# Kernel tuning notes

Hardware: AMD Instinct MI355X
Metric: run time of the kernel (lower is better)

## Reference

```python
import jax, jax.numpy as jnp
import numpy as np

VAR_W = 1.0
DIST_W = 1.0
M_VAR = 0.1
M_DIST = 1.5
IGNORE = 255
C = 16  # static upper bound on instance ids (labels 1..C; 0 = background)


def setup_inputs() -> dict:
    key = jax.random.key(0)
    ks = jax.random.split(key, 6)
    shapes = [(16, 1, 1024, 1024), (16, 1, 512, 512), (16, 1, 256, 256)]
    d = {}
    for idx, s in enumerate(shapes):
        d[f"featmap{idx}"] = jax.random.normal(ks[idx], s, dtype=jnp.float32)
        d[f"gt{idx}"] = jax.random.randint(ks[3 + idx], s, 0, C + 1, dtype=jnp.int32)
    return d


def _push_pull(feats, gts):
    B = feats[0].shape[0]
    nseg = B * (C + 1)
    b_off = (jnp.arange(B, dtype=jnp.int32) * (C + 1))[:, None]  # [B,1]

    segs, valids, ffs = [], [], []
    tot_sum = jnp.zeros((nseg,), dtype=feats[0].dtype)
    tot_cnt = jnp.zeros((nseg,), dtype=feats[0].dtype)
    # pass 1: per (batch, instance) sums / counts pooled over all scales
    for f, g in zip(feats, gts):
        ff = f.reshape(B, -1)            # [B, N_s]
        gg = g.reshape(B, -1)
        valid = (gg >= 1) & (gg <= C) & (gg < IGNORE)
        lab = jnp.where(valid, gg, 0)
        seg = (lab + b_off).reshape(-1)  # [B*N_s], segment id = b*(C+1)+label
        vf = valid.reshape(-1).astype(ff.dtype)
        tot_sum = tot_sum + jax.ops.segment_sum(jnp.where(valid, ff, 0.0).reshape(-1), seg, num_segments=nseg)
        tot_cnt = tot_cnt + jax.ops.segment_sum(vf, seg, num_segments=nseg)
        segs.append(seg); valids.append(valid); ffs.append(ff)

    mean = tot_sum / jnp.maximum(tot_cnt, 1.0)  # [nseg] per-(b,instance) mean over all scales

    # pass 2: pull loss -- per-scale mean of clamp(|x - mean| - margin_var, 0)^2, summed over scales
    pull_seg = jnp.zeros((nseg,), dtype=feats[0].dtype)
    for ff, seg, valid in zip(ffs, segs, valids):
        m_pix = mean[seg].reshape(ff.shape)
        val = jnp.where(valid, jnp.square(jnp.maximum(jnp.abs(ff - m_pix) - M_VAR, 0.0)), 0.0)
        ssum = jax.ops.segment_sum(val.reshape(-1), seg, num_segments=nseg)
        scnt = jax.ops.segment_sum(valid.reshape(-1).astype(ff.dtype), seg, num_segments=nseg)
        pull_seg = pull_seg + jnp.where(scnt > 0, ssum / jnp.maximum(scnt, 1.0), 0.0)

    present = tot_cnt.reshape(B, C + 1)[:, 1:] > 0        # [B,C]
    pull_i = pull_seg.reshape(B, C + 1)[:, 1:]            # [B,C]
    n_pull = jnp.maximum(present.sum(), 1).astype(pull_i.dtype)
    pull_loss = jnp.sum(jnp.where(present, pull_i, 0.0)) / n_pull * VAR_W

    # push loss: all ordered pairs (i,j), i!=j, both present in that batch element
    m = mean.reshape(B, C + 1)[:, 1:]                     # [B,C]
    diff = jnp.abs(m[:, :, None] - m[:, None, :])         # [B,C,C]
    pv = jnp.square(jnp.maximum(2.0 * M_DIST - diff, 0.0))
    pm = present[:, :, None] & present[:, None, :] & ~jnp.eye(C, dtype=bool)[None]
    n_push = jnp.maximum(pm.sum(), 1).astype(pv.dtype)
    push_loss = jnp.sum(jnp.where(pm, pv, 0.0)) / n_push * DIST_W

    return push_loss + pull_loss


def reference(featmap0, featmap1, featmap2, gt0, gt1, gt2):
    return _push_pull([featmap0, featmap1, featmap2], [gt0, gt1, gt2])
```

## Files before the change

kernel.cpp:

```cpp
#include <hip/hip_runtime.h>


#define NSEG 272
#define M_VAR 0.1f
#define TWO_M_DIST 3.0f

__device__ __forceinline__ void gatomic_add(float* p, float v) {
  __hip_atomic_fetch_add(p, v, __ATOMIC_RELAXED, __HIP_MEMORY_SCOPE_AGENT);
}

#define GRID_BLOCKS 1008

struct Sel {
  const float4* f; const int4* g;
  int vbase, vend, stride, scale, batch;
};

__device__ __forceinline__ Sel pick(
    int b, int t,
    const float4* f0, const int4* g0,
    const float4* f1, const int4* g1,
    const float4* f2, const int4* g2) {
  Sel s;
  if (b < 768) {
    int batch = b / 48, sub = b - batch * 48;
    s.f = f0; s.g = g0; s.scale = 0; s.batch = batch;
    s.vbase = batch * 262144 + sub * 256 + t;
    s.vend  = (batch + 1) * 262144;
    s.stride = 48 * 256;
  } else if (b < 960) {
    int lb = b - 768; int batch = lb / 12, sub = lb - batch * 12;
    s.f = f1; s.g = g1; s.scale = 1; s.batch = batch;
    s.vbase = batch * 65536 + sub * 256 + t;
    s.vend  = (batch + 1) * 65536;
    s.stride = 12 * 256;
  } else {
    int lb = b - 960; int batch = lb / 3, sub = lb - batch * 3;
    s.f = f2; s.g = g2; s.scale = 2; s.batch = batch;
    s.vbase = batch * 16384 + sub * 256 + t;
    s.vend  = (batch + 1) * 16384;
    s.stride = 3 * 256;
  }
  return s;
}

__global__ __launch_bounds__(256, 4) void pass1_kernel(
    const float4* __restrict__ f0, const int4* __restrict__ g0,
    const float4* __restrict__ f1, const int4* __restrict__ g1,
    const float4* __restrict__ f2, const int4* __restrict__ g2,
    float* __restrict__ tot_sum,
    float* __restrict__ cnt)
{
  __shared__ float2 bins[17 * 256];
  const int t = threadIdx.x;
  for (int i = t; i < 17 * 256; i += 256) bins[i] = make_float2(0.f, 0.f);
  __syncthreads();

  Sel s = pick(blockIdx.x, t, f0, g0, f1, g1, f2, g2);

  for (int v = s.vbase; v < s.vend; v += s.stride) {
    float4 fv = s.f[v];
    int4   gv = s.g[v];
    {
      int idx = (int)min((unsigned)gv.x, 16u) * 256 + t;
      float2 r = bins[idx]; bins[idx] = make_float2(r.x + fv.x, r.y + 1.f);
    }
    {
      int idx = (int)min((unsigned)gv.y, 16u) * 256 + t;
      float2 r = bins[idx]; bins[idx] = make_float2(r.x + fv.y, r.y + 1.f);
    }
    {
      int idx = (int)min((unsigned)gv.z, 16u) * 256 + t;
      float2 r = bins[idx]; bins[idx] = make_float2(r.x + fv.z, r.y + 1.f);
    }
    {
      int idx = (int)min((unsigned)gv.w, 16u) * 256 + t;
      float2 r = bins[idx]; bins[idx] = make_float2(r.x + fv.w, r.y + 1.f);
    }
  }

  for (int sh = 7; sh >= 0; --sh) {
    __syncthreads();
    int off = 1 << sh;
    for (int i = t; i < 17 * off; i += 256) {
      int l = i >> sh, tt = i & (off - 1);
      int a = l * 256 + tt;
      float2 x = bins[a], y = bins[a + off];
      bins[a] = make_float2(x.x + y.x, x.y + y.y);
    }
  }
  __syncthreads();

  if (t >= 1 && t < 17) {
    float2 r = bins[t * 256];
    if (r.y != 0.f) {
      gatomic_add(&tot_sum[s.batch * 17 + t], r.x);
      gatomic_add(&cnt[s.scale * NSEG + s.batch * 17 + t], r.y);
    }
  }
}

__global__ __launch_bounds__(256) void mean_kernel(
    const float* __restrict__ tot_sum, const float* __restrict__ cnt,
    float* __restrict__ mean, float* __restrict__ tot_cnt) {
  for (int i = threadIdx.x; i < NSEG; i += 256) {
    float c = cnt[i] + cnt[NSEG + i] + cnt[2 * NSEG + i];
    tot_cnt[i] = c;
    mean[i] = tot_sum[i] / fmaxf(c, 1.f);
  }
}

__global__ __launch_bounds__(256, 8) void pass2_kernel(
    const float4* __restrict__ f0, const int4* __restrict__ g0,
    const float4* __restrict__ f1, const int4* __restrict__ g1,
    const float4* __restrict__ f2, const int4* __restrict__ g2,
    const float* __restrict__ mean,
    float* __restrict__ pull)
{
  __shared__ float bins[17 * 256];
  __shared__ float s_mean[17];
  const int t = threadIdx.x;

  Sel s = pick(blockIdx.x, t, f0, g0, f1, g1, f2, g2);

  for (int i = t; i < 17 * 256; i += 256) bins[i] = 0.f;
  if (t < 17) s_mean[t] = mean[s.batch * 17 + t];
  __syncthreads();

  for (int v = s.vbase; v < s.vend; v += s.stride) {
    float4 fv = s.f[v];
    int4   gv = s.g[v];
    {
      int l = (int)min((unsigned)gv.x, 16u);
      float d = fmaxf(fabsf(fv.x - s_mean[l]) - M_VAR, 0.f);
      bins[l * 256 + t] += d * d;
    }
    {
      int l = (int)min((unsigned)gv.y, 16u);
      float d = fmaxf(fabsf(fv.y - s_mean[l]) - M_VAR, 0.f);
      bins[l * 256 + t] += d * d;
    }
    {
      int l = (int)min((unsigned)gv.z, 16u);
      float d = fmaxf(fabsf(fv.z - s_mean[l]) - M_VAR, 0.f);
      bins[l * 256 + t] += d * d;
    }
    {
      int l = (int)min((unsigned)gv.w, 16u);
      float d = fmaxf(fabsf(fv.w - s_mean[l]) - M_VAR, 0.f);
      bins[l * 256 + t] += d * d;
    }
  }

  for (int sh = 7; sh >= 0; --sh) {
    __syncthreads();
    int off = 1 << sh;
    for (int i = t; i < 17 * off; i += 256) {
      int l = i >> sh, tt = i & (off - 1);
      bins[l * 256 + tt] += bins[l * 256 + tt + off];
    }
  }
  __syncthreads();

  if (t >= 1 && t < 17) {
    float r = bins[t * 256];
    if (r != 0.f) gatomic_add(&pull[s.scale * NSEG + s.batch * 17 + t], r);
  }
}

__global__ __launch_bounds__(256) void finalize_kernel(
    const float* __restrict__ tot_cnt, const float* __restrict__ mean,
    const float* __restrict__ cnt, const float* __restrict__ pull,
    float* __restrict__ out) {
  __shared__ float s_mean[NSEG];
  __shared__ unsigned char s_pres[NSEG];
  const int t = threadIdx.x;
  for (int i = t; i < NSEG; i += 256) {
    s_mean[i] = mean[i];
    s_pres[i] = (tot_cnt[i] > 0.f) ? 1 : 0;
  }
  __syncthreads();

  float pull_v = 0.f, pull_n = 0.f, push_v = 0.f, push_n = 0.f;

  for (int i = t; i < NSEG; i += 256) {
    int lab = i - (i / 17) * 17;
    if (lab >= 1 && s_pres[i]) {
      float ps = 0.f;
      float c0 = cnt[i];            if (c0 > 0.f) ps += pull[i] / c0;
      float c1 = cnt[NSEG + i];     if (c1 > 0.f) ps += pull[NSEG + i] / c1;
      float c2 = cnt[2 * NSEG + i]; if (c2 > 0.f) ps += pull[2 * NSEG + i] / c2;
      pull_v += ps;
      pull_n += 1.f;
    }
  }

  {
    int b = t >> 4, ii = t & 15;
    int si = b * 17 + ii + 1;
    if (s_pres[si]) {
      float mi = s_mean[si];
      for (int j = 0; j < 16; ++j) {
        if (j == ii) continue;
        int sj = b * 17 + j + 1;
        if (s_pres[sj]) {
          float d = fmaxf(TWO_M_DIST - fabsf(mi - s_mean[sj]), 0.f);
          push_v += d * d;
          push_n += 1.f;
        }
      }
    }
  }

  #pragma unroll
  for (int o = 32; o > 0; o >>= 1) {
    pull_v += __shfl_down(pull_v, o);
    pull_n += __shfl_down(pull_n, o);
    push_v += __shfl_down(push_v, o);
    push_n += __shfl_down(push_n, o);
  }
  __shared__ float r[4][4];
  int wave = t >> 6;
  if ((t & 63) == 0) { r[wave][0] = pull_v; r[wave][1] = pull_n; r[wave][2] = push_v; r[wave][3] = push_n; }
  __syncthreads();
  if (t == 0) {
    float PV = 0, PN = 0, SV = 0, SN = 0;
    for (int w = 0; w < 4; ++w) { PV += r[w][0]; PN += r[w][1]; SV += r[w][2]; SN += r[w][3]; }
    out[0] = PV / fmaxf(PN, 1.f) + SV / fmaxf(SN, 1.f);
  }
}

extern "C" void kernel_launch(void* const* d_in, const int* in_sizes, int n_in,
                              void* d_out, int out_size, void* d_ws, size_t ws_size,
                              hipStream_t stream) {
  const float4* f0 = (const float4*)d_in[0];
  const int4*   g0 = (const int4*)  d_in[1];
  const float4* f1 = (const float4*)d_in[2];
  const int4*   g1 = (const int4*)  d_in[3];
  const float4* f2 = (const float4*)d_in[4];
  const int4*   g2 = (const int4*)  d_in[5];

  float* ws      = (float*)d_ws;
  float* tot_sum = ws;
  float* cnt     = ws + NSEG;
  float* pull    = ws + 4 * NSEG;
  float* mean    = ws + 7 * NSEG;
  float* tot_cnt = ws + 8 * NSEG;

  hipMemsetAsync(d_ws, 0, 7 * NSEG * sizeof(float), stream);
  pass1_kernel<<<GRID_BLOCKS, 256, 0, stream>>>(f0, g0, f1, g1, f2, g2, tot_sum, cnt);
  mean_kernel<<<1, 256, 0, stream>>>(tot_sum, cnt, mean, tot_cnt);
  pass2_kernel<<<GRID_BLOCKS, 256, 0, stream>>>(f0, g0, f1, g1, f2, g2, mean, pull);
  finalize_kernel<<<1, 256, 0, stream>>>(tot_cnt, mean, cnt, pull, (float*)d_out);
}
```

Measured before the change: 213.9 us.

## Halve LDS histograms with shared atomics, double grid, fold mean kernel into consumers

The per-thread private LDS histograms become 128-column histograms shared by thread pairs and updated with workgroup-scope LDS atomics. This halves LDS per block and allows higher occupancy (launch bound raised to 8 in pass1). The grid doubles (96/24/6 sub-blocks per batch) for more parallelism. The separate mean kernel is removed: pass2 and finalize compute means directly from sums and counts, saving one launch. The cost is LDS atomic contention and atomic instruction overhead in place of plain read-modify-write.

```diff
diff --git a/kernel.cpp b/kernel.cpp
--- a/kernel.cpp
+++ b/kernel.cpp
@@ -5,11 +5,17 @@
 #define M_VAR 0.1f
 #define TWO_M_DIST 3.0f
 
+#define SUB0 96
+#define SUB1 24
+#define SUB2 6
+#define GRID_BLOCKS (16 * (SUB0 + SUB1 + SUB2))
+
 __device__ __forceinline__ void gatomic_add(float* p, float v) {
   __hip_atomic_fetch_add(p, v, __ATOMIC_RELAXED, __HIP_MEMORY_SCOPE_AGENT);
 }
-
-#define GRID_BLOCKS 1008
+__device__ __forceinline__ void latomic_add(float* p, float v) {
+  __hip_atomic_fetch_add(p, v, __ATOMIC_RELAXED, __HIP_MEMORY_SCOPE_WORKGROUP);
+}
 
 struct Sel {
   const float4* f; const int4* g;
@@ -22,91 +28,77 @@
     const float4* f1, const int4* g1,
     const float4* f2, const int4* g2) {
   Sel s;
-  if (b < 768) {
-    int batch = b / 48, sub = b - batch * 48;
+  if (b < 16 * SUB0) {
+    int batch = b / SUB0, sub = b - batch * SUB0;
     s.f = f0; s.g = g0; s.scale = 0; s.batch = batch;
     s.vbase = batch * 262144 + sub * 256 + t;
     s.vend  = (batch + 1) * 262144;
-    s.stride = 48 * 256;
-  } else if (b < 960) {
-    int lb = b - 768; int batch = lb / 12, sub = lb - batch * 12;
+    s.stride = SUB0 * 256;
+  } else if (b < 16 * (SUB0 + SUB1)) {
+    int lb = b - 16 * SUB0; int batch = lb / SUB1, sub = lb - batch * SUB1;
     s.f = f1; s.g = g1; s.scale = 1; s.batch = batch;
     s.vbase = batch * 65536 + sub * 256 + t;
     s.vend  = (batch + 1) * 65536;
-    s.stride = 12 * 256;
+    s.stride = SUB1 * 256;
   } else {
-    int lb = b - 960; int batch = lb / 3, sub = lb - batch * 3;
+    int lb = b - 16 * (SUB0 + SUB1); int batch = lb / SUB2, sub = lb - batch * SUB2;
     s.f = f2; s.g = g2; s.scale = 2; s.batch = batch;
     s.vbase = batch * 16384 + sub * 256 + t;
     s.vend  = (batch + 1) * 16384;
-    s.stride = 3 * 256;
+    s.stride = SUB2 * 256;
   }
   return s;
 }
 
-__global__ __launch_bounds__(256, 4) void pass1_kernel(
+__global__ __launch_bounds__(256, 8) void pass1_kernel(
     const float4* __restrict__ f0, const int4* __restrict__ g0,
     const float4* __restrict__ f1, const int4* __restrict__ g1,
     const float4* __restrict__ f2, const int4* __restrict__ g2,
     float* __restrict__ tot_sum,
     float* __restrict__ cnt)
 {
-  __shared__ float2 bins[17 * 256];
+  __shared__ float ssum[17 * 128];
+  __shared__ float scnt[17 * 128];
   const int t = threadIdx.x;
-  for (int i = t; i < 17 * 256; i += 256) bins[i] = make_float2(0.f, 0.f);
+  for (int i = t; i < 17 * 128; i += 256) { ssum[i] = 0.f; scnt[i] = 0.f; }
   __syncthreads();
 
   Sel s = pick(blockIdx.x, t, f0, g0, f1, g1, f2, g2);
+  const int col = t & 127;
+  float* bs = ssum + col;
+  float* bc = scnt + col;
 
   for (int v = s.vbase; v < s.vend; v += s.stride) {
     float4 fv = s.f[v];
     int4   gv = s.g[v];
-    {
-      int idx = (int)min((unsigned)gv.x, 16u) * 256 + t;
-      float2 r = bins[idx]; bins[idx] = make_float2(r.x + fv.x, r.y + 1.f);
-    }
-    {
-      int idx = (int)min((unsigned)gv.y, 16u) * 256 + t;
-      float2 r = bins[idx]; bins[idx] = make_float2(r.x + fv.y, r.y + 1.f);
-    }
-    {
-      int idx = (int)min((unsigned)gv.z, 16u) * 256 + t;
-      float2 r = bins[idx]; bins[idx] = make_float2(r.x + fv.z, r.y + 1.f);
-    }
-    {
-      int idx = (int)min((unsigned)gv.w, 16u) * 256 + t;
-      float2 r = bins[idx]; bins[idx] = make_float2(r.x + fv.w, r.y + 1.f);
-    }
-  }
-
-  for (int sh = 7; sh >= 0; --sh) {
+    int lx = (int)min((unsigned)gv.x, 16u);
+    int ly = (int)min((unsigned)gv.y, 16u);
+    int lz = (int)min((unsigned)gv.z, 16u);
+    int lw = (int)min((unsigned)gv.w, 16u);
+    latomic_add(bs + lx * 128, fv.x);  latomic_add(bc + lx * 128, 1.f);
+    latomic_add(bs + ly * 128, fv.y);  latomic_add(bc + ly * 128, 1.f);
+    latomic_add(bs + lz * 128, fv.z);  latomic_add(bc + lz * 128, 1.f);
+    latomic_add(bs + lw * 128, fv.w);  latomic_add(bc + lw * 128, 1.f);
+  }
+
+  for (int sh = 6; sh >= 0; --sh) {
     __syncthreads();
     int off = 1 << sh;
     for (int i = t; i < 17 * off; i += 256) {
-      int l = i >> sh, tt = i & (off - 1);
-      int a = l * 256 + tt;
-      float2 x = bins[a], y = bins[a + off];
-      bins[a] = make_float2(x.x + y.x, x.y + y.y);
+      int l = i >> sh, c = i & (off - 1);
+      int a = l * 128 + c;
+      ssum[a] += ssum[a + off];
+      scnt[a] += scnt[a + off];
     }
   }
   __syncthreads();
 
   if (t >= 1 && t < 17) {
-    float2 r = bins[t * 256];
-    if (r.y != 0.f) {
-      gatomic_add(&tot_sum[s.batch * 17 + t], r.x);
-      gatomic_add(&cnt[s.scale * NSEG + s.batch * 17 + t], r.y);
-    }
-  }
-}
-
-__global__ __launch_bounds__(256) void mean_kernel(
-    const float* __restrict__ tot_sum, const float* __restrict__ cnt,
-    float* __restrict__ mean, float* __restrict__ tot_cnt) {
-  for (int i = threadIdx.x; i < NSEG; i += 256) {
-    float c = cnt[i] + cnt[NSEG + i] + cnt[2 * NSEG + i];
-    tot_cnt[i] = c;
-    mean[i] = tot_sum[i] / fmaxf(c, 1.f);
+    float cv = scnt[t * 128];
+    if (cv != 0.f) {
+      gatomic_add(&tot_sum[s.batch * 17 + t], ssum[t * 128]);
+      gatomic_add(&cnt[s.scale * NSEG + s.batch * 17 + t], cv);
+    }
   }
 }
 
@@ -114,18 +106,26 @@
     const float4* __restrict__ f0, const int4* __restrict__ g0,
     const float4* __restrict__ f1, const int4* __restrict__ g1,
     const float4* __restrict__ f2, const int4* __restrict__ g2,
-    const float* __restrict__ mean,
+    const float* __restrict__ tot_sum,
+    const float* __restrict__ cnt,
     float* __restrict__ pull)
 {
-  __shared__ float bins[17 * 256];
+  __shared__ float bins[17 * 128];
   __shared__ float s_mean[17];
   const int t = threadIdx.x;
 
   Sel s = pick(blockIdx.x, t, f0, g0, f1, g1, f2, g2);
 
-  for (int i = t; i < 17 * 256; i += 256) bins[i] = 0.f;
-  if (t < 17) s_mean[t] = mean[s.batch * 17 + t];
-  __syncthreads();
+  for (int i = t; i < 17 * 128; i += 256) bins[i] = 0.f;
+  if (t < 17) {
+    int i = s.batch * 17 + t;
+    float c = cnt[i] + cnt[NSEG + i] + cnt[2 * NSEG + i];
+    s_mean[t] = tot_sum[i] / fmaxf(c, 1.f);
+  }
+  __syncthreads();
+
+  const int col = t & 127;
+  float* bb = bins + col;
 
   for (int v = s.vbase; v < s.vend; v += s.stride) {
     float4 fv = s.f[v];
@@ -133,51 +133,52 @@
     {
       int l = (int)min((unsigned)gv.x, 16u);
       float d = fmaxf(fabsf(fv.x - s_mean[l]) - M_VAR, 0.f);
-      bins[l * 256 + t] += d * d;
+      latomic_add(bb + l * 128, d * d);
     }
     {
       int l = (int)min((unsigned)gv.y, 16u);
       float d = fmaxf(fabsf(fv.y - s_mean[l]) - M_VAR, 0.f);
-      bins[l * 256 + t] += d * d;
+      latomic_add(bb + l * 128, d * d);
     }
     {
       int l = (int)min((unsigned)gv.z, 16u);
       float d = fmaxf(fabsf(fv.z - s_mean[l]) - M_VAR, 0.f);
-      bins[l * 256 + t] += d * d;
+      latomic_add(bb + l * 128, d * d);
     }
     {
       int l = (int)min((unsigned)gv.w, 16u);
       float d = fmaxf(fabsf(fv.w - s_mean[l]) - M_VAR, 0.f);
-      bins[l * 256 + t] += d * d;
-    }
-  }
-
-  for (int sh = 7; sh >= 0; --sh) {
+      latomic_add(bb + l * 128, d * d);
+    }
+  }
+
+  for (int sh = 6; sh >= 0; --sh) {
     __syncthreads();
     int off = 1 << sh;
     for (int i = t; i < 17 * off; i += 256) {
-      int l = i >> sh, tt = i & (off - 1);
-      bins[l * 256 + tt] += bins[l * 256 + tt + off];
+      int l = i >> sh, c = i & (off - 1);
+      bins[l * 128 + c] += bins[l * 128 + c + off];
     }
   }
   __syncthreads();
 
   if (t >= 1 && t < 17) {
-    float r = bins[t * 256];
+    float r = bins[t * 128];
     if (r != 0.f) gatomic_add(&pull[s.scale * NSEG + s.batch * 17 + t], r);
   }
 }
 
 __global__ __launch_bounds__(256) void finalize_kernel(
-    const float* __restrict__ tot_cnt, const float* __restrict__ mean,
+    const float* __restrict__ tot_sum,
     const float* __restrict__ cnt, const float* __restrict__ pull,
     float* __restrict__ out) {
   __shared__ float s_mean[NSEG];
   __shared__ unsigned char s_pres[NSEG];
   const int t = threadIdx.x;
   for (int i = t; i < NSEG; i += 256) {
-    s_mean[i] = mean[i];
-    s_pres[i] = (tot_cnt[i] > 0.f) ? 1 : 0;
+    float c = cnt[i] + cnt[NSEG + i] + cnt[2 * NSEG + i];
+    s_pres[i] = (c > 0.f) ? 1 : 0;
+    s_mean[i] = tot_sum[i] / fmaxf(c, 1.f);
   }
   __syncthreads();
 
@@ -244,12 +245,9 @@
   float* tot_sum = ws;
   float* cnt     = ws + NSEG;
   float* pull    = ws + 4 * NSEG;
-  float* mean    = ws + 7 * NSEG;
-  float* tot_cnt = ws + 8 * NSEG;
 
   hipMemsetAsync(d_ws, 0, 7 * NSEG * sizeof(float), stream);
   pass1_kernel<<<GRID_BLOCKS, 256, 0, stream>>>(f0, g0, f1, g1, f2, g2, tot_sum, cnt);
-  mean_kernel<<<1, 256, 0, stream>>>(tot_sum, cnt, mean, tot_cnt);
-  pass2_kernel<<<GRID_BLOCKS, 256, 0, stream>>>(f0, g0, f1, g1, f2, g2, mean, pull);
-  finalize_kernel<<<1, 256, 0, stream>>>(tot_cnt, mean, cnt, pull, (float*)d_out);
-}
+  pass2_kernel<<<GRID_BLOCKS, 256, 0, stream>>>(f0, g0, f1, g1, f2, g2, tot_sum, cnt, pull);
+  finalize_kernel<<<1, 256, 0, stream>>>(tot_sum, cnt, pull, (float*)d_out);
+}
```

Result: slower. 475.1 us (+122.1%).
